# Kernel tuning notes

Measured on AMD Instinct MI355X. Metric: run time of the kernel, lower is better.

## Reference

```python
import jax, jax.numpy as jnp
import numpy as np

N_NODES = 100000
N_EDGES = 1000000
D_IN = 128
D_H = 128
N_CLS = 16


def setup_inputs() -> dict:
    key = jax.random.key(0)
    ks = jax.random.split(key, 12)
    s_in = 1.0 / np.sqrt(D_IN)
    s_h = 1.0 / np.sqrt(D_H)
    s_2h = 1.0 / np.sqrt(2 * D_H)
    return {
        "x": jax.random.normal(ks[0], (N_NODES, D_IN), jnp.float32),
        "edge_index": jax.random.randint(ks[1], (2, N_EDGES), 0, N_NODES, jnp.int64),
        "W_l0": jax.random.normal(ks[2], (D_H, D_IN), jnp.float32) * s_in,
        "b_l0": jnp.zeros((D_H,), jnp.float32),
        "W_r0": jax.random.normal(ks[3], (D_H, D_IN), jnp.float32) * s_in,
        "W_l1": jax.random.normal(ks[4], (D_H, D_H), jnp.float32) * s_h,
        "b_l1": jnp.zeros((D_H,), jnp.float32),
        "W_r1": jax.random.normal(ks[5], (D_H, D_H), jnp.float32) * s_h,
        "W_c": jax.random.normal(ks[6], (D_H, 2 * D_H), jnp.float32) * s_2h,
        "b_c": jnp.zeros((D_H,), jnp.float32),
        "W_o": jax.random.normal(ks[7], (N_CLS, 2 * D_H), jnp.float32) * s_2h,
        "b_o": jnp.zeros((N_CLS,), jnp.float32),
    }


def _sage_conv(x, src, dst, W_l, b_l, W_r, num_nodes):
    # PyG SAGEConv (mean aggr): lin_l(mean of source-neighbor feats) + lin_r(x)
    msgs = x[src]  # [E, d] gather
    agg = jax.ops.segment_sum(msgs, dst, num_segments=num_nodes)
    cnt = jax.ops.segment_sum(jnp.ones((src.shape[0],), x.dtype), dst, num_segments=num_nodes)
    mean = agg / jnp.maximum(cnt, 1.0)[:, None]
    return mean @ W_l.T + b_l + x @ W_r.T


def reference(x, edge_index, W_l0, b_l0, W_r0, W_l1, b_l1, W_r1, W_c, b_c, W_o, b_o):
    src, dst = edge_index[0], edge_index[1]
    n = x.shape[0]
    for W_l, b_l, W_r in ((W_l0, b_l0, W_r0), (W_l1, b_l1, W_r1)):
        x_old = x
        h = jax.nn.relu(_sage_conv(x, src, dst, W_l, b_l, W_r, n))
        x = jnp.concatenate([x_old, h], axis=-1)  # [N, 2*hidden]
        x = jax.nn.relu(x @ W_c.T + b_c)
        # dropout: identity (eval mode)
    edge_feats = jnp.concatenate([x[src], x[dst]], axis=-1)  # [E, 2*hidden]
    return edge_feats @ W_o.T + b_o
```

## Files before the change

kernel.cpp:

```cpp
#include <hip/hip_runtime.h>
#include <hip/hip_bf16.h>

#define NN 100000
#define NE 1000000
#define D  128
#define NC 16

typedef short short8 __attribute__((ext_vector_type(8)));
typedef float f32x4  __attribute__((ext_vector_type(4)));

__device__ __forceinline__ float bf2f(ushort u) {
  union { unsigned int i; float f; } v; v.i = ((unsigned int)u) << 16; return v.f;
}
__device__ __forceinline__ ushort f2bf(float f) {
  union { float f; unsigned int i; } v; v.f = f;
  unsigned int x = v.i;
  return (ushort)((x + 0x7FFFu + ((x >> 16) & 1u)) >> 16);
}

#define BSH 9
#define NBKT ((NN + 511) >> BSH)
#define MS_NBLK 256
#define MS_EPB ((NE + MS_NBLK - 1) / MS_NBLK)
#define CSR_CAP 8192

__global__ void sniff_k(const ushort* __restrict__ xr, const unsigned int* __restrict__ ei,
                        int* __restrict__ flags, int* __restrict__ bhist) {
  int t = threadIdx.x;
  if (t < NBKT) bhist[t] = 0;
  if (t != 0 || blockIdx.x != 0) return;
  int f32 = 0;
  for (int i = 0; i < 128; ++i) {
    unsigned int e = ((unsigned int)xr[i] >> 7) & 0xFFu;
    if (e < 97u || e > 157u) f32 = 1;
  }
  flags[0] = f32;
  unsigned int s = 0;
  for (int i = 1; i < 256; i += 2) s |= ei[i];
  flags[1] = (s == 0) ? 1 : 0;
}

__global__ __launch_bounds__(256) void convert_idx_k(
    const int* __restrict__ ei, const int* __restrict__ flags,
    int* __restrict__ idx, int* __restrict__ bhist) {
  __shared__ int h[NBKT];
  for (int t = threadIdx.x; t < NBKT; t += 256) h[t] = 0;
  __syncthreads();
  const int stride = 256 * 256;
  const int i64 = flags[1];
  for (int i = blockIdx.x * 256 + threadIdx.x; i < 2 * NE; i += stride) {
    int v = i64 ? ei[2 * i] : ei[i];
    v = v < 0 ? 0 : (v >= NN ? NN - 1 : v);
    idx[i] = v;
    if (i >= NE) atomicAdd(&h[v >> BSH], 1);
  }
  __syncthreads();
  for (int t = threadIdx.x; t < NBKT; t += 256) if (h[t]) atomicAdd(&bhist[t], h[t]);
}

__global__ void convert_x_k(const void* __restrict__ xin, const int* __restrict__ flags,
                            ushort* __restrict__ xb) {
  int i = blockIdx.x * blockDim.x + threadIdx.x;
  const int n4 = NN * D / 4;
  if (i >= n4) return;
  ushort4 o;
  if (flags[0]) {
    float4 v = ((const float4*)xin)[i];
    o.x = f2bf(v.x); o.y = f2bf(v.y); o.z = f2bf(v.z); o.w = f2bf(v.w);
  } else {
    o = ((const ushort4*)xin)[i];
  }
  ((ushort4*)xb)[i] = o;
}

struct WPtrs { const void* p[10]; };
#define WTOT 102800
__global__ void convert_w_k(WPtrs w, const int* __restrict__ flags, ushort* __restrict__ wb) {
  const int off[10] = {0, 16384, 32768, 49152, 65536, 98304, 102400, 102528, 102656, 102784};
  int i = blockIdx.x * blockDim.x + threadIdx.x;
  if (i >= WTOT) return;
  int seg = 0;
  #pragma unroll
  for (int s2 = 1; s2 < 10; ++s2) if (i >= off[s2]) seg = s2;
  int j = i - off[seg];
  wb[i] = flags[0] ? f2bf(((const float*)w.p[seg])[j]) : ((const ushort*)w.p[seg])[j];
}

__global__ __launch_bounds__(256) void scanb_k(const int* __restrict__ bhist,
                                               int* __restrict__ bstart,
                                               int* __restrict__ bcur) {
  __shared__ int tmp[256];
  const int t = threadIdx.x;
  int v = (t < NBKT) ? bhist[t] : 0;
  tmp[t] = v;
  __syncthreads();
  for (int s = 1; s < 256; s <<= 1) {
    int u = (t >= s) ? tmp[t - s] : 0;
    __syncthreads();
    tmp[t] += u;
    __syncthreads();
  }
  if (t < NBKT) {
    int ex = tmp[t] - v;
    bstart[t] = ex;
    bcur[t] = ex;
  }
  if (t == NBKT - 1) bstart[NBKT] = tmp[t];
}

__global__ __launch_bounds__(512) void msplit_k(const int* __restrict__ src,
                                                const int* __restrict__ dst,
                                                int* __restrict__ bcur,
                                                int2* __restrict__ ebuf) {
  __shared__ int2 ep[MS_EPB];
  __shared__ int hist[NBKT];
  __shared__ int gbase[NBKT];
  const int e0 = blockIdx.x * MS_EPB;
  int n = NE - e0; if (n > MS_EPB) n = MS_EPB;
  for (int t = threadIdx.x; t < NBKT; t += 512) hist[t] = 0;
  __syncthreads();
  for (int t = threadIdx.x; t < n; t += 512) {
    int s = src[e0 + t], d = dst[e0 + t];
    ep[t] = make_int2(s, d);
    atomicAdd(&hist[d >> BSH], 1);
  }
  __syncthreads();
  for (int t = threadIdx.x; t < NBKT; t += 512) {
    gbase[t] = atomicAdd(&bcur[t], hist[t]);
    hist[t] = 0;
  }
  __syncthreads();
  for (int t = threadIdx.x; t < n; t += 512) {
    int2 p = ep[t];
    int b = p.y >> BSH;
    int loc = atomicAdd(&hist[b], 1);
    ebuf[gbase[b] + loc] = p;
  }
}

__global__ __launch_bounds__(512) void csr_k(const int2* __restrict__ ebuf,
                                             const int* __restrict__ bstart,
                                             int* __restrict__ off,
                                             int* __restrict__ nbr) {
  __shared__ int cnt_s[512];
  __shared__ int ofs_s[512];
  __shared__ int lnbr[CSR_CAP];
  const int b = blockIdx.x;
  const int n0 = b << BSH;
  int nn = NN - n0; if (nn > 512) nn = 512;
  const int e0 = bstart[b], e1 = bstart[b + 1];
  const int n = e1 - e0;
  const int t = threadIdx.x;
  cnt_s[t] = 0;
  __syncthreads();
  for (int i = t; i < n; i += 512)
    atomicAdd(&cnt_s[ebuf[e0 + i].y - n0], 1);
  __syncthreads();
  int v = cnt_s[t];
  ofs_s[t] = v;
  __syncthreads();
  for (int s = 1; s < 512; s <<= 1) {
    int u = (t >= s) ? ofs_s[t - s] : 0;
    __syncthreads();
    ofs_s[t] += u;
    __syncthreads();
  }
  const int excl = ofs_s[t] - v;
  if (t < nn) off[n0 + t] = e0 + excl;
  if (b == gridDim.x - 1 && t == 0) off[NN] = e1;
  cnt_s[t] = excl;
  __syncthreads();
  if (n <= CSR_CAP) {
    for (int i = t; i < n; i += 512) {
      int2 p = ebuf[e0 + i];
      int loc = atomicAdd(&cnt_s[p.y - n0], 1);
      lnbr[loc] = p.x;
    }
    __syncthreads();
    for (int i = t; i < n; i += 512) nbr[e0 + i] = lnbr[i];
  } else {
    for (int i = t; i < n; i += 512) {
      int2 p = ebuf[e0 + i];
      int loc = atomicAdd(&cnt_s[p.y - n0], 1);
      nbr[e0 + loc] = p.x;
    }
  }
}

__global__ __launch_bounds__(256) void agg_k(
    const ushort* __restrict__ X, const int* __restrict__ nbr,
    const int* __restrict__ off, ushort* __restrict__ mean) {
  const int wave = threadIdx.x >> 6, lane = threadIdx.x & 63;
  const int node = blockIdx.x * 4 + wave;
  if (node >= NN) return;
  const int j0 = off[node], j1 = off[node + 1];
  const int g = lane >> 4, l15 = lane & 15;
  float a[8];
  #pragma unroll
  for (int k = 0; k < 8; ++k) a[k] = 0.f;
  int j = j0 + g;
  for (; j + 4 < j1; j += 8) {
    int s0 = nbr[j], s1 = nbr[j + 4];
    uint4 v0 = *(const uint4*)(X + (size_t)s0 * D + l15 * 8);
    uint4 v1 = *(const uint4*)(X + (size_t)s1 * D + l15 * 8);
    unsigned int w0[4] = {v0.x, v0.y, v0.z, v0.w};
    unsigned int w1[4] = {v1.x, v1.y, v1.z, v1.w};
    #pragma unroll
    for (int k = 0; k < 4; ++k) {
      union { unsigned int u; float f; } lo0, hi0, lo1, hi1;
      lo0.u = w0[k] << 16; hi0.u = w0[k] & 0xffff0000u;
      lo1.u = w1[k] << 16; hi1.u = w1[k] & 0xffff0000u;
      a[2 * k]     += lo0.f + lo1.f;
      a[2 * k + 1] += hi0.f + hi1.f;
    }
  }
  if (j < j1) {
    uint4 v0 = *(const uint4*)(X + (size_t)nbr[j] * D + l15 * 8);
    unsigned int w0[4] = {v0.x, v0.y, v0.z, v0.w};
    #pragma unroll
    for (int k = 0; k < 4; ++k) {
      union { unsigned int u; float f; } lo0, hi0;
      lo0.u = w0[k] << 16; hi0.u = w0[k] & 0xffff0000u;
      a[2 * k]     += lo0.f;
      a[2 * k + 1] += hi0.f;
    }
  }
  #pragma unroll
  for (int k = 0; k < 8; ++k) {
    a[k] += __shfl_xor(a[k], 16, 64);
    a[k] += __shfl_xor(a[k], 32, 64);
  }
  if (g == 0) {
    int deg = j1 - j0;
    float inv = 1.f / (float)(deg > 1 ? deg : 1);
    uint4 o;
    o.x = (unsigned int)f2bf(a[0] * inv) | ((unsigned int)f2bf(a[1] * inv) << 16);
    o.y = (unsigned int)f2bf(a[2] * inv) | ((unsigned int)f2bf(a[3] * inv) << 16);
    o.z = (unsigned int)f2bf(a[4] * inv) | ((unsigned int)f2bf(a[5] * inv) << 16);
    o.w = (unsigned int)f2bf(a[6] * inv) | ((unsigned int)f2bf(a[7] * inv) << 16);
    *(uint4*)(mean + (size_t)node * D + l15 * 8) = o;
  }
}

#define STAGE_WH(Wp, ldwv, HALF)                                               \
  __syncthreads();                                                             \
  _Pragma("unroll")                                                            \
  for (int it = 0; it < 4; ++it) {                                             \
    int combo = it * 4 + wave;                                                 \
    int cc = combo >> 2, kk = combo & 3;                                       \
    *(uint4*)(&wlds[(combo * 64 + lane) * 8]) =                                \
        *(const uint4*)((Wp) + (size_t)(((HALF) * 4 + cc) * 16 + l15) * (ldwv) + kk * 32 + q * 8); \
  }                                                                            \
  __syncthreads();

#define MFMA_HALF(bfr, HALF)                                                   \
  _Pragma("unroll")                                                            \
  for (int ks = 0; ks < 4; ++ks)                                               \
    _Pragma("unroll")                                                          \
    for (int cl = 0; cl < 4; ++cl) {                                           \
      short8 bf = *(const short8*)(&wlds[((cl * 4 + ks) * 64 + lane) * 8]);    \
      acc[0][(HALF) * 4 + cl] =                                                \
          __builtin_amdgcn_mfma_f32_16x16x32_bf16(bf, (bfr)[0][ks], acc[0][(HALF) * 4 + cl], 0, 0, 0); \
      acc[1][(HALF) * 4 + cl] =                                                \
          __builtin_amdgcn_mfma_f32_16x16x32_bf16(bf, (bfr)[1][ks], acc[1][(HALF) * 4 + cl], 0, 0, 0); \
    }

#define MFMA_HHALF(HALF)                                                       \
  _Pragma("unroll")                                                            \
  for (int ks = 0; ks < 4; ++ks) {                                             \
    short8 h0 = *(const short8*)(&hlds[hb0 + ks * 32 + q * 8]);                \
    short8 h1 = *(const short8*)(&hlds[hb1 + ks * 32 + q * 8]);                \
    _Pragma("unroll")                                                          \
    for (int cl = 0; cl < 4; ++cl) {                                           \
      short8 bf = *(const short8*)(&wlds[((cl * 4 + ks) * 64 + lane) * 8]);    \
      acc[0][(HALF) * 4 + cl] =                                                \
          __builtin_amdgcn_mfma_f32_16x16x32_bf16(bf, h0, acc[0][(HALF) * 4 + cl], 0, 0, 0); \
      acc[1][(HALF) * 4 + cl] =                                                \
          __builtin_amdgcn_mfma_f32_16x16x32_bf16(bf, h1, acc[1][(HALF) * 4 + cl], 0, 0, 0); \
    }                                                                          \
  }

#define HLDW 132

__global__ __launch_bounds__(256, 2) void fused_layer_k(
    const ushort* __restrict__ MEAN, const ushort* __restrict__ X,
    const ushort* __restrict__ Wl, const ushort* __restrict__ Wr,
    const ushort* __restrict__ Wc,
    const ushort* __restrict__ bl, const ushort* __restrict__ bc,
    ushort* __restrict__ Y, int nrows)
{
  __shared__ ushort wlds[16 * 64 * 8];
  __shared__ ushort hlds[128 * HLDW];
  const int tid = threadIdx.x;
  const int wave = tid >> 6, lane = tid & 63;
  const int l15 = lane & 15, q = lane >> 4;
  const int nb = blockIdx.x * 128 + wave * 32;

  int r0 = nb + l15;      if (r0 > nrows - 1) r0 = nrows - 1;
  int r1 = nb + 16 + l15; if (r1 > nrows - 1) r1 = nrows - 1;

  short8 am[2][4], ax[2][4];
  #pragma unroll
  for (int ks = 0; ks < 4; ++ks) {
    am[0][ks] = *(const short8*)(MEAN + (size_t)r0 * D + ks * 32 + q * 8);
    am[1][ks] = *(const short8*)(MEAN + (size_t)r1 * D + ks * 32 + q * 8);
    ax[0][ks] = *(const short8*)(X    + (size_t)r0 * D + ks * 32 + q * 8);
    ax[1][ks] = *(const short8*)(X    + (size_t)r1 * D + ks * 32 + q * 8);
  }

  f32x4 acc[2][8];
  #pragma unroll
  for (int rt = 0; rt < 2; ++rt)
    #pragma unroll
    for (int c = 0; c < 8; ++c) acc[rt][c] = (f32x4){0.f, 0.f, 0.f, 0.f};

  STAGE_WH(Wl, D, 0);  MFMA_HALF(am, 0);
  STAGE_WH(Wl, D, 1);  MFMA_HALF(am, 1);
  STAGE_WH(Wr, D, 0);  MFMA_HALF(ax, 0);
  STAGE_WH(Wr, D, 1);  MFMA_HALF(ax, 1);

  #pragma unroll
  for (int c = 0; c < 8; ++c) {
    ushort4 bv = *(const ushort4*)(bl + c * 16 + q * 4);
    #pragma unroll
    for (int rt = 0; rt < 2; ++rt) {
      float v0 = acc[rt][c][0] + bf2f(bv.x); v0 = v0 > 0.f ? v0 : 0.f;
      float v1 = acc[rt][c][1] + bf2f(bv.y); v1 = v1 > 0.f ? v1 : 0.f;
      float v2 = acc[rt][c][2] + bf2f(bv.z); v2 = v2 > 0.f ? v2 : 0.f;
      float v3 = acc[rt][c][3] + bf2f(bv.w); v3 = v3 > 0.f ? v3 : 0.f;
      uint2 o;
      o.x = (unsigned int)f2bf(v0) | ((unsigned int)f2bf(v1) << 16);
      o.y = (unsigned int)f2bf(v2) | ((unsigned int)f2bf(v3) << 16);
      int nl = wave * 32 + rt * 16 + l15;
      *(uint2*)(&hlds[nl * HLDW + c * 16 + q * 4]) = o;
    }
  }

  #pragma unroll
  for (int rt = 0; rt < 2; ++rt)
    #pragma unroll
    for (int c = 0; c < 8; ++c) acc[rt][c] = (f32x4){0.f, 0.f, 0.f, 0.f};

  const int hb0 = (wave * 32 + l15) * HLDW;
  const int hb1 = (wave * 32 + 16 + l15) * HLDW;

  STAGE_WH(Wc, 2 * D, 0);      MFMA_HALF(ax, 0);
  STAGE_WH(Wc, 2 * D, 1);      MFMA_HALF(ax, 1);
  STAGE_WH(Wc + D, 2 * D, 0);  MFMA_HHALF(0);
  STAGE_WH(Wc + D, 2 * D, 1);  MFMA_HHALF(1);

  #pragma unroll
  for (int c = 0; c < 8; ++c) {
    ushort4 bv = *(const ushort4*)(bc + c * 16 + q * 4);
    #pragma unroll
    for (int rt = 0; rt < 2; ++rt) {
      int node = nb + rt * 16 + l15;
      if (node < nrows) {
        float v0 = acc[rt][c][0] + bf2f(bv.x); v0 = v0 > 0.f ? v0 : 0.f;
        float v1 = acc[rt][c][1] + bf2f(bv.y); v1 = v1 > 0.f ? v1 : 0.f;
        float v2 = acc[rt][c][2] + bf2f(bv.z); v2 = v2 > 0.f ? v2 : 0.f;
        float v3 = acc[rt][c][3] + bf2f(bv.w); v3 = v3 > 0.f ? v3 : 0.f;
        uint2 o;
        o.x = (unsigned int)f2bf(v0) | ((unsigned int)f2bf(v1) << 16);
        o.y = (unsigned int)f2bf(v2) | ((unsigned int)f2bf(v3) << 16);
        *(uint2*)(Y + (size_t)node * D + c * 16 + q * 4) = o;
      }
    }
  }
}

__global__ __launch_bounds__(256) void gemm_po(
    const ushort* __restrict__ X2, const ushort* __restrict__ Wo, float* __restrict__ P)
{
  const int tid = threadIdx.x, wave = tid >> 6, lane = tid & 63;
  const int l15 = lane & 15, q = lane >> 4;
  const int m0 = blockIdx.x * 64 + wave * 16;
  int row = m0 + l15; if (row > NN - 1) row = NN - 1;
  f32x4 acc[2] = {(f32x4){0.f,0.f,0.f,0.f}, (f32x4){0.f,0.f,0.f,0.f}};
  #pragma unroll
  for (int ks = 0; ks < 4; ++ks) {
    short8 af = *(const short8*)(X2 + (size_t)row * D + ks * 32 + q * 8);
    #pragma unroll
    for (int c = 0; c < 2; ++c) {
      short8 bf = *(const short8*)(Wo + (size_t)l15 * 256 + c * 128 + ks * 32 + q * 8);
      acc[c] = __builtin_amdgcn_mfma_f32_16x16x32_bf16(af, bf, acc[c], 0, 0, 0);
    }
  }
  #pragma unroll
  for (int c = 0; c < 2; ++c)
    #pragma unroll
    for (int r = 0; r < 4; ++r) {
      int orow = m0 + q * 4 + r;
      if (orow < NN) P[(size_t)orow * 32 + c * 16 + l15] = acc[c][r];
    }
}

__global__ __launch_bounds__(256) void edge_sum_k(
    const float* __restrict__ P, const int* __restrict__ src, const int* __restrict__ dst,
    const ushort* __restrict__ bo, const int* __restrict__ flags,
    void* __restrict__ outv, int E)
{
  int gid = blockIdx.x * blockDim.x + threadIdx.x;
  if (gid >= E * 4) return;
  int e = gid >> 2, cq = (gid & 3) * 4;
  int s = src[e], d = dst[e];
  float4 a = *(const float4*)(P + (size_t)s * 32 + cq);
  float4 b = *(const float4*)(P + (size_t)d * 32 + 16 + cq);
  float4 o;
  o.x = a.x + b.x + bf2f(bo[cq + 0]);
  o.y = a.y + b.y + bf2f(bo[cq + 1]);
  o.z = a.z + b.z + bf2f(bo[cq + 2]);
  o.w = a.w + b.w + bf2f(bo[cq + 3]);
  if (flags[0]) {
    ((float4*)outv)[gid] = o;
  } else {
    ushort4 u;
    u.x = f2bf(o.x); u.y = f2bf(o.y); u.z = f2bf(o.z); u.w = f2bf(o.w);
    ((ushort4*)outv)[gid] = u;
  }
}

extern "C" void kernel_launch(void* const* d_in, const int* in_sizes, int n_in,
                              void* d_out, int out_size, void* d_ws, size_t ws_size,
                              hipStream_t stream) {
  const void* x_in = d_in[0];
  const int*  ei   = (const int*)d_in[1];

  char* ws = (char*)d_ws;
  int*    idx   = (int*)(ws + 0);
  int*    bhist = (int*)(ws + 8000000);
  int*    flags = (int*)(ws + 8400000);
  ushort* wb    = (ushort*)(ws + 8400256);
  int*    off   = (int*)(ws + 8605856);
  int*    bstart= (int*)(ws + 9005872);
  int*    nbr   = (int*)(ws + 9405872);
  int*    bcur  = (int*)(ws + 13405872);
  ushort* buf1  = (ushort*)(ws + 13407440);
  ushort* buf2  = (ushort*)(ws + 39007440);
  ushort* dscr  = (ushort*)d_out;
  float*  P     = (float*)buf1;
  int2*   ebuf  = (int2*)buf1;

  int* src = idx;
  int* dst = idx + NE;

  ushort* Wl0 = wb + 0,      *Wr0 = wb + 16384, *Wl1 = wb + 32768, *Wr1 = wb + 49152;
  ushort* Wc  = wb + 65536,  *Wo  = wb + 98304;
  ushort* bl0 = wb + 102400, *bl1 = wb + 102528, *bc = wb + 102656, *bo = wb + 102784;

  WPtrs w;
  w.p[0] = d_in[2];  w.p[1] = d_in[4];  w.p[2] = d_in[5];  w.p[3] = d_in[7];
  w.p[4] = d_in[8];  w.p[5] = d_in[10]; w.p[6] = d_in[3];  w.p[7] = d_in[6];
  w.p[8] = d_in[9];  w.p[9] = d_in[11];

  const int gblocks = (NN + 127) / 128;
  const int n4 = NN * D / 4;
  const int agrid = (NN + 3) / 4;

  sniff_k<<<1, 256, 0, stream>>>((const ushort*)x_in, (const unsigned int*)ei, flags, bhist);
  convert_idx_k<<<256, 256, 0, stream>>>(ei, flags, idx, bhist);
  convert_x_k<<<(n4 + 255) / 256, 256, 0, stream>>>(x_in, flags, buf2);
  convert_w_k<<<(WTOT + 255) / 256, 256, 0, stream>>>(w, flags, wb);

  scanb_k<<<1, 256, 0, stream>>>(bhist, bstart, bcur);
  msplit_k<<<MS_NBLK, 512, 0, stream>>>(src, dst, bcur, ebuf);
  csr_k<<<NBKT, 512, 0, stream>>>(ebuf, bstart, off, nbr);

  agg_k<<<agrid, 256, 0, stream>>>(buf2, nbr, off, dscr);
  fused_layer_k<<<gblocks, 256, 0, stream>>>(dscr, buf2, Wl0, Wr0, Wc, bl0, bc, buf1, NN);

  agg_k<<<agrid, 256, 0, stream>>>(buf1, nbr, off, dscr);
  fused_layer_k<<<gblocks, 256, 0, stream>>>(dscr, buf1, Wl1, Wr1, Wc, bl1, bc, buf2, NN);

  gemm_po<<<(NN + 63) / 64, 256, 0, stream>>>(buf2, Wo, P);
  edge_sum_k<<<(4 * NE + 255) / 256, 256, 0, stream>>>(P, src, dst, bo, flags, d_out, NE);
}
```

Before: 436.1 us.

## Prefetch weight tiles into registers during MFMA and prescale neighbor indices

The fused layer kernel now loads the next weight half-tile from global memory into registers while the current tile's MFMAs run, then commits it to LDS after a barrier. Before, each stage did the global load and LDS store together between barriers, so the load latency was exposed. The CSR build stores neighbor indices pre-multiplied by the row stride (128), which removes a multiply from the aggregation gather's address math. Launch bounds are raised to 3 blocks per SM, which limits registers even though the extra prefetch registers increase pressure.

```diff
diff --git a/kernel.cpp b/kernel.cpp
--- a/kernel.cpp
+++ b/kernel.cpp
@@ -174,7 +174,7 @@
     for (int i = t; i < n; i += 512) {
       int2 p = ebuf[e0 + i];
       int loc = atomicAdd(&cnt_s[p.y - n0], 1);
-      lnbr[loc] = p.x;
+      lnbr[loc] = p.x << 7;
     }
     __syncthreads();
     for (int i = t; i < n; i += 512) nbr[e0 + i] = lnbr[i];
@@ -182,7 +182,7 @@
     for (int i = t; i < n; i += 512) {
       int2 p = ebuf[e0 + i];
       int loc = atomicAdd(&cnt_s[p.y - n0], 1);
-      nbr[e0 + loc] = p.x;
+      nbr[e0 + loc] = p.x << 7;
     }
   }
 }
@@ -201,8 +201,8 @@
   int j = j0 + g;
   for (; j + 4 < j1; j += 8) {
     int s0 = nbr[j], s1 = nbr[j + 4];
-    uint4 v0 = *(const uint4*)(X + (size_t)s0 * D + l15 * 8);
-    uint4 v1 = *(const uint4*)(X + (size_t)s1 * D + l15 * 8);
+    uint4 v0 = *(const uint4*)(X + (size_t)(unsigned)s0 + l15 * 8);
+    uint4 v1 = *(const uint4*)(X + (size_t)(unsigned)s1 + l15 * 8);
     unsigned int w0[4] = {v0.x, v0.y, v0.z, v0.w};
     unsigned int w1[4] = {v1.x, v1.y, v1.z, v1.w};
     #pragma unroll
@@ -215,7 +215,7 @@
     }
   }
   if (j < j1) {
-    uint4 v0 = *(const uint4*)(X + (size_t)nbr[j] * D + l15 * 8);
+    uint4 v0 = *(const uint4*)(X + (size_t)(unsigned)nbr[j] + l15 * 8);
     unsigned int w0[4] = {v0.x, v0.y, v0.z, v0.w};
     #pragma unroll
     for (int k = 0; k < 4; ++k) {
@@ -242,14 +242,20 @@
   }
 }
 
-#define STAGE_WH(Wp, ldwv, HALF)                                               \
+#define ISSUE_W(Wp, ldwv, HALF)                                                \
+  _Pragma("unroll")                                                            \
+  for (int it = 0; it < 4; ++it) {                                             \
+    int combo = it * 4 + wave;                                                 \
+    int cc = combo >> 2, kk = combo & 3;                                       \
+    pf[it] = *(const uint4*)((Wp) + (size_t)(((HALF) * 4 + cc) * 16 + l15) * (ldwv) + kk * 32 + q * 8); \
+  }
+
+#define COMMIT_W()                                                             \
   __syncthreads();                                                             \
   _Pragma("unroll")                                                            \
   for (int it = 0; it < 4; ++it) {                                             \
     int combo = it * 4 + wave;                                                 \
-    int cc = combo >> 2, kk = combo & 3;                                       \
-    *(uint4*)(&wlds[(combo * 64 + lane) * 8]) =                                \
-        *(const uint4*)((Wp) + (size_t)(((HALF) * 4 + cc) * 16 + l15) * (ldwv) + kk * 32 + q * 8); \
+    *(uint4*)(&wlds[(combo * 64 + lane) * 8]) = pf[it];                        \
   }                                                                            \
   __syncthreads();
 
@@ -282,7 +288,7 @@
 
 #define HLDW 132
 
-__global__ __launch_bounds__(256, 2) void fused_layer_k(
+__global__ __launch_bounds__(256, 3) void fused_layer_k(
     const ushort* __restrict__ MEAN, const ushort* __restrict__ X,
     const ushort* __restrict__ Wl, const ushort* __restrict__ Wr,
     const ushort* __restrict__ Wc,
@@ -314,10 +320,13 @@
     #pragma unroll
     for (int c = 0; c < 8; ++c) acc[rt][c] = (f32x4){0.f, 0.f, 0.f, 0.f};
 
-  STAGE_WH(Wl, D, 0);  MFMA_HALF(am, 0);
-  STAGE_WH(Wl, D, 1);  MFMA_HALF(am, 1);
-  STAGE_WH(Wr, D, 0);  MFMA_HALF(ax, 0);
-  STAGE_WH(Wr, D, 1);  MFMA_HALF(ax, 1);
+  uint4 pf[4];
+
+  ISSUE_W(Wl, D, 0);
+  COMMIT_W();  ISSUE_W(Wl, D, 1);      MFMA_HALF(am, 0);
+  COMMIT_W();  ISSUE_W(Wr, D, 0);      MFMA_HALF(am, 1);
+  COMMIT_W();  ISSUE_W(Wr, D, 1);      MFMA_HALF(ax, 0);
+  COMMIT_W();  ISSUE_W(Wc, 2 * D, 0);  MFMA_HALF(ax, 1);
 
   #pragma unroll
   for (int c = 0; c < 8; ++c) {
@@ -335,7 +344,6 @@
       *(uint2*)(&hlds[nl * HLDW + c * 16 + q * 4]) = o;
     }
   }
-
   #pragma unroll
   for (int rt = 0; rt < 2; ++rt)
     #pragma unroll
@@ -344,10 +352,10 @@
   const int hb0 = (wave * 32 + l15) * HLDW;
   const int hb1 = (wave * 32 + 16 + l15) * HLDW;
 
-  STAGE_WH(Wc, 2 * D, 0);      MFMA_HALF(ax, 0);
-  STAGE_WH(Wc, 2 * D, 1);      MFMA_HALF(ax, 1);
-  STAGE_WH(Wc + D, 2 * D, 0);  MFMA_HHALF(0);
-  STAGE_WH(Wc + D, 2 * D, 1);  MFMA_HHALF(1);
+  COMMIT_W();  ISSUE_W(Wc, 2 * D, 1);      MFMA_HALF(ax, 0);
+  COMMIT_W();  ISSUE_W(Wc + D, 2 * D, 0);  MFMA_HALF(ax, 1);
+  COMMIT_W();  ISSUE_W(Wc + D, 2 * D, 1);  MFMA_HHALF(0);
+  COMMIT_W();                              MFMA_HHALF(1);
 
   #pragma unroll
   for (int c = 0; c < 8; ++c) {
```

Measured after the change: 466.2 us. 1.07x slower.

## Fuse output projection into second layer kernel and merge scan with weight conversion

Applied to the files above, without the earlier changes.

The second fused layer kernel now stages its relu output in LDS and runs the Wo projection directly, writing the per-node P scores and skipping both the bf16 store of the layer-2 activations and the separate gemm_po launch with its reload. The bucket scan and weight conversion are merged into one launch. CSR neighbor indices are stored pre-multiplied by the row stride so agg_k skips a multiply per gather. This adds LDS traffic and register pressure to fused_layer_k, and the pre-shifted indices assume node*128 fits in 32 bits.

```diff
diff --git a/kernel.cpp b/kernel.cpp
--- a/kernel.cpp
+++ b/kernel.cpp
@@ -75,37 +75,37 @@
 
 struct WPtrs { const void* p[10]; };
 #define WTOT 102800
-__global__ void convert_w_k(WPtrs w, const int* __restrict__ flags, ushort* __restrict__ wb) {
-  const int off[10] = {0, 16384, 32768, 49152, 65536, 98304, 102400, 102528, 102656, 102784};
-  int i = blockIdx.x * blockDim.x + threadIdx.x;
-  if (i >= WTOT) return;
-  int seg = 0;
-  #pragma unroll
-  for (int s2 = 1; s2 < 10; ++s2) if (i >= off[s2]) seg = s2;
-  int j = i - off[seg];
-  wb[i] = flags[0] ? f2bf(((const float*)w.p[seg])[j]) : ((const ushort*)w.p[seg])[j];
-}
-
-__global__ __launch_bounds__(256) void scanb_k(const int* __restrict__ bhist,
-                                               int* __restrict__ bstart,
-                                               int* __restrict__ bcur) {
-  __shared__ int tmp[256];
-  const int t = threadIdx.x;
-  int v = (t < NBKT) ? bhist[t] : 0;
-  tmp[t] = v;
-  __syncthreads();
-  for (int s = 1; s < 256; s <<= 1) {
-    int u = (t >= s) ? tmp[t - s] : 0;
+__global__ __launch_bounds__(256) void scan_convw_k(
+    const int* __restrict__ bhist, int* __restrict__ bstart, int* __restrict__ bcur,
+    WPtrs w, const int* __restrict__ flags, ushort* __restrict__ wb) {
+  if (blockIdx.x == 0) {
+    __shared__ int tmp[256];
+    const int t = threadIdx.x;
+    int v = (t < NBKT) ? bhist[t] : 0;
+    tmp[t] = v;
     __syncthreads();
-    tmp[t] += u;
-    __syncthreads();
-  }
-  if (t < NBKT) {
-    int ex = tmp[t] - v;
-    bstart[t] = ex;
-    bcur[t] = ex;
-  }
-  if (t == NBKT - 1) bstart[NBKT] = tmp[t];
+    for (int s = 1; s < 256; s <<= 1) {
+      int u = (t >= s) ? tmp[t - s] : 0;
+      __syncthreads();
+      tmp[t] += u;
+      __syncthreads();
+    }
+    if (t < NBKT) {
+      int ex = tmp[t] - v;
+      bstart[t] = ex;
+      bcur[t] = ex;
+    }
+    if (t == NBKT - 1) bstart[NBKT] = tmp[t];
+  } else {
+    const int off[10] = {0, 16384, 32768, 49152, 65536, 98304, 102400, 102528, 102656, 102784};
+    int i = (blockIdx.x - 1) * 256 + threadIdx.x;
+    if (i >= WTOT) return;
+    int seg = 0;
+    #pragma unroll
+    for (int s2 = 1; s2 < 10; ++s2) if (i >= off[s2]) seg = s2;
+    int j = i - off[seg];
+    wb[i] = flags[0] ? f2bf(((const float*)w.p[seg])[j]) : ((const ushort*)w.p[seg])[j];
+  }
 }
 
 __global__ __launch_bounds__(512) void msplit_k(const int* __restrict__ src,
@@ -174,7 +174,7 @@
     for (int i = t; i < n; i += 512) {
       int2 p = ebuf[e0 + i];
       int loc = atomicAdd(&cnt_s[p.y - n0], 1);
-      lnbr[loc] = p.x;
+      lnbr[loc] = p.x << 7;
     }
     __syncthreads();
     for (int i = t; i < n; i += 512) nbr[e0 + i] = lnbr[i];
@@ -182,7 +182,7 @@
     for (int i = t; i < n; i += 512) {
       int2 p = ebuf[e0 + i];
       int loc = atomicAdd(&cnt_s[p.y - n0], 1);
-      nbr[e0 + loc] = p.x;
+      nbr[e0 + loc] = p.x << 7;
     }
   }
 }
@@ -201,8 +201,8 @@
   int j = j0 + g;
   for (; j + 4 < j1; j += 8) {
     int s0 = nbr[j], s1 = nbr[j + 4];
-    uint4 v0 = *(const uint4*)(X + (size_t)s0 * D + l15 * 8);
-    uint4 v1 = *(const uint4*)(X + (size_t)s1 * D + l15 * 8);
+    uint4 v0 = *(const uint4*)(X + (size_t)(unsigned)s0 + l15 * 8);
+    uint4 v1 = *(const uint4*)(X + (size_t)(unsigned)s1 + l15 * 8);
     unsigned int w0[4] = {v0.x, v0.y, v0.z, v0.w};
     unsigned int w1[4] = {v1.x, v1.y, v1.z, v1.w};
     #pragma unroll
@@ -215,7 +215,7 @@
     }
   }
   if (j < j1) {
-    uint4 v0 = *(const uint4*)(X + (size_t)nbr[j] * D + l15 * 8);
+    uint4 v0 = *(const uint4*)(X + (size_t)(unsigned)nbr[j] + l15 * 8);
     unsigned int w0[4] = {v0.x, v0.y, v0.z, v0.w};
     #pragma unroll
     for (int k = 0; k < 4; ++k) {
@@ -286,8 +286,9 @@
     const ushort* __restrict__ MEAN, const ushort* __restrict__ X,
     const ushort* __restrict__ Wl, const ushort* __restrict__ Wr,
     const ushort* __restrict__ Wc,
+    const ushort* __restrict__ Wo,
     const ushort* __restrict__ bl, const ushort* __restrict__ bc,
-    ushort* __restrict__ Y, int nrows)
+    ushort* __restrict__ Y, float* __restrict__ P, int nrows)
 {
   __shared__ ushort wlds[16 * 64 * 8];
   __shared__ ushort hlds[128 * HLDW];
@@ -349,50 +350,53 @@
   STAGE_WH(Wc + D, 2 * D, 0);  MFMA_HHALF(0);
   STAGE_WH(Wc + D, 2 * D, 1);  MFMA_HHALF(1);
 
+  const bool doP = (P != nullptr);
   #pragma unroll
   for (int c = 0; c < 8; ++c) {
     ushort4 bv = *(const ushort4*)(bc + c * 16 + q * 4);
     #pragma unroll
     for (int rt = 0; rt < 2; ++rt) {
       int node = nb + rt * 16 + l15;
-      if (node < nrows) {
-        float v0 = acc[rt][c][0] + bf2f(bv.x); v0 = v0 > 0.f ? v0 : 0.f;
-        float v1 = acc[rt][c][1] + bf2f(bv.y); v1 = v1 > 0.f ? v1 : 0.f;
-        float v2 = acc[rt][c][2] + bf2f(bv.z); v2 = v2 > 0.f ? v2 : 0.f;
-        float v3 = acc[rt][c][3] + bf2f(bv.w); v3 = v3 > 0.f ? v3 : 0.f;
-        uint2 o;
-        o.x = (unsigned int)f2bf(v0) | ((unsigned int)f2bf(v1) << 16);
-        o.y = (unsigned int)f2bf(v2) | ((unsigned int)f2bf(v3) << 16);
+      float v0 = acc[rt][c][0] + bf2f(bv.x); v0 = v0 > 0.f ? v0 : 0.f;
+      float v1 = acc[rt][c][1] + bf2f(bv.y); v1 = v1 > 0.f ? v1 : 0.f;
+      float v2 = acc[rt][c][2] + bf2f(bv.z); v2 = v2 > 0.f ? v2 : 0.f;
+      float v3 = acc[rt][c][3] + bf2f(bv.w); v3 = v3 > 0.f ? v3 : 0.f;
+      uint2 o;
+      o.x = (unsigned int)f2bf(v0) | ((unsigned int)f2bf(v1) << 16);
+      o.y = (unsigned int)f2bf(v2) | ((unsigned int)f2bf(v3) << 16);
+      if (doP) {
+        int nl = wave * 32 + rt * 16 + l15;
+        *(uint2*)(&hlds[nl * HLDW + c * 16 + q * 4]) = o;
+      } else if (node < nrows) {
         *(uint2*)(Y + (size_t)node * D + c * 16 + q * 4) = o;
       }
     }
   }
-}
-
-__global__ __launch_bounds__(256) void gemm_po(
-    const ushort* __restrict__ X2, const ushort* __restrict__ Wo, float* __restrict__ P)
-{
-  const int tid = threadIdx.x, wave = tid >> 6, lane = tid & 63;
-  const int l15 = lane & 15, q = lane >> 4;
-  const int m0 = blockIdx.x * 64 + wave * 16;
-  int row = m0 + l15; if (row > NN - 1) row = NN - 1;
-  f32x4 acc[2] = {(f32x4){0.f,0.f,0.f,0.f}, (f32x4){0.f,0.f,0.f,0.f}};
-  #pragma unroll
-  for (int ks = 0; ks < 4; ++ks) {
-    short8 af = *(const short8*)(X2 + (size_t)row * D + ks * 32 + q * 8);
-    #pragma unroll
-    for (int c = 0; c < 2; ++c) {
-      short8 bf = *(const short8*)(Wo + (size_t)l15 * 256 + c * 128 + ks * 32 + q * 8);
-      acc[c] = __builtin_amdgcn_mfma_f32_16x16x32_bf16(af, bf, acc[c], 0, 0, 0);
-    }
-  }
-  #pragma unroll
-  for (int c = 0; c < 2; ++c)
-    #pragma unroll
-    for (int r = 0; r < 4; ++r) {
-      int orow = m0 + q * 4 + r;
-      if (orow < NN) P[(size_t)orow * 32 + c * 16 + l15] = acc[c][r];
-    }
+
+  if (doP) {
+    #pragma unroll
+    for (int rt = 0; rt < 2; ++rt) {
+      f32x4 ap0 = (f32x4){0.f, 0.f, 0.f, 0.f};
+      f32x4 ap1 = (f32x4){0.f, 0.f, 0.f, 0.f};
+      const int hb = (wave * 32 + rt * 16 + l15) * HLDW;
+      #pragma unroll
+      for (int ks = 0; ks < 4; ++ks) {
+        short8 af = *(const short8*)(&hlds[hb + ks * 32 + q * 8]);
+        short8 b0 = *(const short8*)(Wo + (size_t)l15 * 256 + ks * 32 + q * 8);
+        short8 b1 = *(const short8*)(Wo + (size_t)l15 * 256 + 128 + ks * 32 + q * 8);
+        ap0 = __builtin_amdgcn_mfma_f32_16x16x32_bf16(af, b0, ap0, 0, 0, 0);
+        ap1 = __builtin_amdgcn_mfma_f32_16x16x32_bf16(af, b1, ap1, 0, 0, 0);
+      }
+      #pragma unroll
+      for (int r = 0; r < 4; ++r) {
+        int node = nb + rt * 16 + q * 4 + r;
+        if (node < nrows) {
+          P[(size_t)node * 32 + l15]      = ap0[r];
+          P[(size_t)node * 32 + 16 + l15] = ap1[r];
+        }
+      }
+    }
+  }
 }
 
 __global__ __launch_bounds__(256) void edge_sum_k(
@@ -438,8 +442,8 @@
   ushort* buf1  = (ushort*)(ws + 13407440);
   ushort* buf2  = (ushort*)(ws + 39007440);
   ushort* dscr  = (ushort*)d_out;
-  float*  P     = (float*)buf1;
   int2*   ebuf  = (int2*)buf1;
+  float*  P     = (float*)buf2;
 
   int* src = idx;
   int* dst = idx + NE;
@@ -460,18 +464,18 @@
   sniff_k<<<1, 256, 0, stream>>>((const ushort*)x_in, (const unsigned int*)ei, flags, bhist);
   convert_idx_k<<<256, 256, 0, stream>>>(ei, flags, idx, bhist);
   convert_x_k<<<(n4 + 255) / 256, 256, 0, stream>>>(x_in, flags, buf2);
-  convert_w_k<<<(WTOT + 255) / 256, 256, 0, stream>>>(w, flags, wb);
-
-  scanb_k<<<1, 256, 0, stream>>>(bhist, bstart, bcur);
+
+  scan_convw_k<<<1 + (WTOT + 255) / 256, 256, 0, stream>>>(bhist, bstart, bcur, w, flags, wb);
   msplit_k<<<MS_NBLK, 512, 0, stream>>>(src, dst, bcur, ebuf);
   csr_k<<<NBKT, 512, 0, stream>>>(ebuf, bstart, off, nbr);
 
   agg_k<<<agrid, 256, 0, stream>>>(buf2, nbr, off, dscr);
-  fused_layer_k<<<gblocks, 256, 0, stream>>>(dscr, buf2, Wl0, Wr0, Wc, bl0, bc, buf1, NN);
+  fused_layer_k<<<gblocks, 256, 0, stream>>>(dscr, buf2, Wl0, Wr0, Wc, Wo, bl0, bc,
+                                             buf1, nullptr, NN);
 
   agg_k<<<agrid, 256, 0, stream>>>(buf1, nbr, off, dscr);
-  fused_layer_k<<<gblocks, 256, 0, stream>>>(dscr, buf1, Wl1, Wr1, Wc, bl1, bc, buf2, NN);
-
-  gemm_po<<<(NN + 63) / 64, 256, 0, stream>>>(buf2, Wo, P);
+  fused_layer_k<<<gblocks, 256, 0, stream>>>(dscr, buf1, Wl1, Wr1, Wc, Wo, bl1, bc,
+                                             nullptr, P, NN);
+
   edge_sum_k<<<(4 * NE + 255) / 256, 256, 0, stream>>>(P, src, dst, bo, flags, d_out, NE);
 }
```

New measurement: 417.2 us. 1.05x faster.
